# Optimization experiments

Hardware: AMD Instinct MI355X
Metric: run time of the kernel (lower is better)

Reference implementation:

```python
import jax, jax.numpy as jnp
import numpy as np

N_NODES = 100000
N_EDGES = 3200000
NEG_SLOPE = 0.2  # PyG GATConv default


def _gat_conv(x, src, dst, W, a_src, a_dst, b, num_nodes):
    # x: [N, Fin]; src/dst: [E'] (self-loops already appended)
    h = x @ W                                   # [N, Fout]
    alpha_src = h @ a_src                       # [N]
    alpha_dst = h @ a_dst                       # [N]
    e = jax.nn.leaky_relu(alpha_src[src] + alpha_dst[dst], NEG_SLOPE)  # [E']
    # segment softmax over incoming edges of each destination node
    e_max = jax.ops.segment_max(e, dst, num_segments=num_nodes)
    e_exp = jnp.exp(e - e_max[dst])
    denom = jax.ops.segment_sum(e_exp, dst, num_segments=num_nodes)
    alpha = e_exp / (denom[dst] + 1e-16)        # [E']
    out = jax.ops.segment_sum(h[src] * alpha[:, None], dst, num_segments=num_nodes)
    return out + b


def setup_inputs() -> dict:
    key = jax.random.key(0)
    ks = jax.random.split(key, 10)
    x = jax.random.normal(ks[0], (N_NODES, 1), jnp.float32)
    edge_index = jax.random.randint(ks[1], (2, N_EDGES), 0, N_NODES, dtype=jnp.int64)
    s1 = 1.0  # glorot-ish scales
    return {
        "x": x,
        "edge_index": edge_index,
        "W1": jax.random.normal(ks[2], (1, 20), jnp.float32) * s1,
        "a_src1": jax.random.normal(ks[3], (20,), jnp.float32) * 0.3,
        "a_dst1": jax.random.normal(ks[4], (20,), jnp.float32) * 0.3,
        "b1": jnp.zeros((20,), jnp.float32),
        "W2": jax.random.normal(ks[5], (20, 20), jnp.float32) * (1.0 / np.sqrt(20.0)),
        "a_src2": jax.random.normal(ks[6], (20,), jnp.float32) * 0.3,
        "a_dst2": jax.random.normal(ks[7], (20,), jnp.float32) * 0.3,
        "b2": jnp.zeros((20,), jnp.float32),
        "Wl": jax.random.normal(ks[8], (20, 1), jnp.float32) * (1.0 / np.sqrt(20.0)),
        "bl": jnp.zeros((1,), jnp.float32),
    }


def reference(x, edge_index, W1, a_src1, a_dst1, b1, W2, a_src2, a_dst2, b2, Wl, bl):
    n = x.shape[0]
    loop = jnp.arange(n, dtype=edge_index.dtype)
    src = jnp.concatenate([edge_index[0], loop])  # add_self_loops=True
    dst = jnp.concatenate([edge_index[1], loop])
    h = _gat_conv(x, src, dst, W1, a_src1, a_dst1, b1, n)
    h = jax.nn.relu(h)
    h = _gat_conv(h, src, dst, W2, a_src2, a_dst2, b2, n)
    h = jax.nn.relu(h)
    return h @ Wl + bl  # [N, 1]
```

## Files before the change

kernel.cpp:

```cpp
#include <hip/hip_runtime.h>
#include <hip/hip_fp16.h>

#define FDIM 20
#define NSLOPE 0.2f
#define BSHIFT 7
#define BSIZE 128
#define BCAP 4800
#define MAXBUCK 800
#define PGRID 512
#define HSTRIDE 24
#define ABLK 512
#define ITP 4
#define CHCAP 6272
#define OFFSTRIDE 132

__device__ __forceinline__ float lrelu(float v) { return v > 0.f ? v : NSLOPE * v; }

__global__ void __launch_bounds__(1024)
k_part(const int* __restrict__ ei, int E, int nbuck,
       const float* __restrict__ x, const float* __restrict__ W1,
       const float* __restrict__ a_src, const float* __restrict__ a_dst,
       float2* __restrict__ PX, float* __restrict__ AD,
       int* __restrict__ gcur, int* __restrict__ slab, int N)
{
    __shared__ int hist[MAXBUCK];
    __shared__ int lofs[MAXBUCK];
    __shared__ int gbase[MAXBUCK];
    __shared__ int sbuf[CHCAP];
    __shared__ unsigned short sbk[CHCAP];
    __shared__ int wsum[16];
    const int tid = threadIdx.x;

    {
        int g = blockIdx.x * 1024 + tid;
        if (g < N) {
            float cs = 0.f, cd = 0.f;
#pragma unroll
            for (int f = 0; f < FDIM; ++f) {
                float w = W1[f]; cs += w * a_src[f]; cd += w * a_dst[f];
            }
            float xv = x[g];
            PX[g] = make_float2(xv * cs, xv);
            AD[g] = xv * cd;
        }
    }

    const int chunk = (E + PGRID - 1) / PGRID;
    const int c0 = blockIdx.x * chunk;
    const int c1 = min(c0 + chunk, E);
    for (int t = tid; t < nbuck; t += 1024) hist[t] = 0;
    __syncthreads();

    int ent[2 * ITP], meta[2 * ITP];
#pragma unroll
    for (int it = 0; it < ITP; ++it) {
        int i = c0 + 2 * (tid + (it << 10));
        const int k0 = 2 * it, k1 = 2 * it + 1;
        meta[k0] = -1; meta[k1] = -1;
        if (i + 1 < c1) {
            int2 s2 = *(const int2*)(ei + i);
            int2 d2 = *(const int2*)(ei + E + i);
            int bA = d2.x >> BSHIFT, bB = d2.y >> BSHIFT;
            int lpA = atomicAdd(&hist[bA], 1);
            int lpB = atomicAdd(&hist[bB], 1);
            ent[k0]  = (s2.x << BSHIFT) | (d2.x & (BSIZE - 1));
            meta[k0] = (lpA << 10) | bA;
            ent[k1]  = (s2.y << BSHIFT) | (d2.y & (BSIZE - 1));
            meta[k1] = (lpB << 10) | bB;
        } else if (i < c1) {
            int s = ei[i], d = ei[E + i];
            int b = d >> BSHIFT;
            int lp = atomicAdd(&hist[b], 1);
            ent[k0]  = (s << BSHIFT) | (d & (BSIZE - 1));
            meta[k0] = (lp << 10) | b;
        }
    }
    __syncthreads();

    int myc = 0;
    if (tid < nbuck) {
        myc = hist[tid];
        gbase[tid] = myc ? atomicAdd(gcur + tid, myc) : 0;
    }
    int inc = myc;
#pragma unroll
    for (int o = 1; o < 64; o <<= 1) {
        int t = __shfl_up(inc, o);
        if ((tid & 63) >= o) inc += t;
    }
    if ((tid & 63) == 63) wsum[tid >> 6] = inc;
    __syncthreads();
    if (tid < 16) {
        int v = wsum[tid];
        int e = v;
#pragma unroll
        for (int o = 1; o < 16; o <<= 1) {
            int t = __shfl_up(e, o);
            if (tid >= o) e += t;
        }
        wsum[tid] = e - v;
    }
    __syncthreads();
    if (tid < nbuck) lofs[tid] = inc - myc + wsum[tid >> 6];
    __syncthreads();

#pragma unroll
    for (int k = 0; k < 2 * ITP; ++k) {
        int m = meta[k];
        if (m >= 0) {
            int b  = m & 1023;
            int lp = m >> 10;
            int pos = lofs[b] + lp;
            sbuf[pos] = ent[k];
            sbk[pos]  = (unsigned short)b;
        }
    }
    __syncthreads();

    const int cnt = c1 - c0;
    for (int i = tid; i < cnt; i += 1024) {
        int b  = sbk[i];
        int gp = gbase[b] + (i - lofs[b]);
        if (gp < BCAP) slab[(size_t)b * BCAP + gp] = sbuf[i];
    }
}

__device__ __forceinline__ void sort_bucket(const int* __restrict__ sp, int cnt,
                                            int* __restrict__ sedge,
                                            int* __restrict__ off,
                                            int* __restrict__ cur)
{
    const int tid = threadIdx.x;
    if (tid < BSIZE + 1) off[tid] = 0;
    __syncthreads();
    for (int i = tid; i < cnt; i += ABLK)
        atomicAdd(&off[(sp[i] & (BSIZE - 1)) + 1], 1);
    __syncthreads();
    if (tid < 64) {
        int a = off[2 * tid + 1];
        int c = off[2 * tid + 2];
        int s = a + c;
#pragma unroll
        for (int o = 1; o < 64; o <<= 1) {
            int t = __shfl_up(s, o);
            if (tid >= o) s += t;
        }
        int ex = s - a - c;
        off[2 * tid]     = ex;
        off[2 * tid + 1] = ex + a;
        cur[2 * tid]     = ex;
        cur[2 * tid + 1] = ex + a;
        if (tid == 63) off[BSIZE] = s;
    }
    __syncthreads();
    for (int i = tid; i < cnt; i += ABLK) {
        int e = sp[i];
        int pos = atomicAdd(&cur[e & (BSIZE - 1)], 1);
        sedge[pos] = e >> BSHIFT;
    }
    __syncthreads();
}

__global__ void __launch_bounds__(ABLK)
k_agg1(const int* __restrict__ gcur, const int* __restrict__ slab,
       const float2* __restrict__ PX, const float* __restrict__ AD,
       const float* __restrict__ W1, const float* __restrict__ b1,
       const float* __restrict__ W2,
       const float* __restrict__ as2w, const float* __restrict__ ad2w,
       __half* __restrict__ H, float* __restrict__ AD2,
       int* __restrict__ sedge_g, int* __restrict__ off_g, int N)
{
    __shared__ int sedge[BCAP];
    __shared__ int off[BSIZE + 1], cur[BSIZE];
    __shared__ float sAD[BSIZE];
    __shared__ float sW1[FDIM], sb1[FDIM], sW2[FDIM * FDIM], sas[FDIM], sad[FDIM];
    const int tid = threadIdx.x;
    const int b = blockIdx.x;
    const int dbase = b << BSHIFT;
    if (tid < BSIZE) { int d = dbase + tid; sAD[tid] = (d < N) ? AD[d] : 0.f; }
    for (int t = tid; t < FDIM * FDIM; t += ABLK) sW2[t] = W2[t];
    if (tid >= 480 && tid < 480 + FDIM) {
        int k = tid - 480;
        sW1[k] = W1[k]; sb1[k] = b1[k]; sas[k] = as2w[k]; sad[k] = ad2w[k];
    }
    const int cnt = min(gcur[b], BCAP);
    sort_bucket(slab + (size_t)b * BCAP, cnt, sedge, off, cur);

    for (int i = tid; i < cnt; i += ABLK) sedge_g[(size_t)b * BCAP + i] = sedge[i];
    if (tid <= BSIZE) off_g[b * OFFSTRIDE + tid] = off[tid];

    const int dl = tid >> 2, sub = tid & 3;
    const float adv = sAD[dl];
    float den = 0.f, sx = 0.f;
    const int e1 = off[dl + 1];
#pragma unroll 4
    for (int j = off[dl] + sub; j < e1; j += 4) {
        int s = sedge[j];
        float2 p = PX[s];
        float w = __expf(lrelu(p.x + adv));
        den += w; sx += w * p.y;
    }
    den += __shfl_xor(den, 1); den += __shfl_xor(den, 2);
    sx  += __shfl_xor(sx, 1);  sx  += __shfl_xor(sx, 2);
    const int d = dbase + dl;
    if (d < N) {
        float2 p = PX[d];
        float w = __expf(lrelu(p.x + adv));
        den += w; sx += w * p.y;
        float sv = sx / (den + 1e-16f);
        float tk[FDIM];
#pragma unroll
        for (int k = 0; k < FDIM; ++k) {
            float tv = sv * sW1[k] + sb1[k];
            tk[k] = tv > 0.f ? tv : 0.f;
        }
        const int fbase = sub << 3;
        const int nf = (sub < 2) ? 8 : (sub == 2 ? 4 : 0);
        float hv[8];
        float pas = 0.f, pad = 0.f;
#pragma unroll
        for (int t = 0; t < 8; ++t) {
            float hsum = 0.f;
            if (t < nf) {
#pragma unroll
                for (int k = 0; k < FDIM; ++k)
                    hsum += tk[k] * sW2[k * FDIM + fbase + t];
                pas += hsum * sas[fbase + t];
                pad += hsum * sad[fbase + t];
            }
            hv[t] = hsum;
        }
        pas += __shfl_xor(pas, 1); pas += __shfl_xor(pas, 2);
        pad += __shfl_xor(pad, 1); pad += __shfl_xor(pad, 2);
        __half2 p01 = __halves2half2(__float2half(hv[0]), __float2half(hv[1]));
        __half2 p23 = __halves2half2(__float2half(hv[2]), __float2half(hv[3]));
        __half2 p45 = __halves2half2(__float2half(hv[4]), __float2half(hv[5]));
        __half2 p67 = __halves2half2(__float2half(hv[6]), __float2half(hv[7]));
        uint4 q;
        q.x = *(unsigned*)&p01; q.y = *(unsigned*)&p23;
        q.z = *(unsigned*)&p45; q.w = *(unsigned*)&p67;
        if (sub == 2) { q.z = __float_as_uint(pas); q.w = 0u; }
        if (sub < 3) ((uint4*)(H + (size_t)d * HSTRIDE))[sub] = q;
        else AD2[d] = pad;
    }
}

__global__ void __launch_bounds__(ABLK)
k_agg2(const int* __restrict__ gcur, const int* __restrict__ sedge_g,
       const int* __restrict__ off_g,
       const __half* __restrict__ H, const float* __restrict__ AD2,
       const float* __restrict__ b2, const float* __restrict__ Wl,
       const float* __restrict__ bl,
       float* __restrict__ out, int N)
{
    __shared__ int sedge[BCAP];
    __shared__ int off[BSIZE + 1];
    __shared__ float sAD[BSIZE];
    __shared__ float sb2[FDIM], sWl[FDIM];
    const int tid = threadIdx.x;
    const int b = blockIdx.x;
    const int dbase = b << BSHIFT;
    if (tid < BSIZE) { int d = dbase + tid; sAD[tid] = (d < N) ? AD2[d] : 0.f; }
    if (tid >= 480 && tid < 480 + FDIM) {
        int k = tid - 480;
        sb2[k] = b2[k]; sWl[k] = Wl[k];
    }
    const int cnt = min(gcur[b], BCAP);
    for (int i = tid; i < cnt; i += ABLK) sedge[i] = sedge_g[(size_t)b * BCAP + i];
    if (tid <= BSIZE) off[tid] = off_g[b * OFFSTRIDE + tid];
    __syncthreads();

    const int dl = tid >> 2, sub = tid & 3;
    const float adv = sAD[dl];
    float den = 0.f;
    float acc[FDIM];
#pragma unroll
    for (int k = 0; k < FDIM; ++k) acc[k] = 0.f;
    const int e1 = off[dl + 1];
#pragma unroll 4
    for (int j = off[dl] + sub; j < e1; j += 4) {
        int s = sedge[j];
        const uint4* rp = (const uint4*)(H + (size_t)s * HSTRIDE);
        uint4 a = rp[0];
        uint4 bb = rp[1];
        uint4 c = rp[2];
        float w = __expf(lrelu(__uint_as_float(c.z) + adv));
        den += w;
        float2 f;
        f = __half22float2(*(__half2*)&a.x);  acc[0]  += w * f.x; acc[1]  += w * f.y;
        f = __half22float2(*(__half2*)&a.y);  acc[2]  += w * f.x; acc[3]  += w * f.y;
        f = __half22float2(*(__half2*)&a.z);  acc[4]  += w * f.x; acc[5]  += w * f.y;
        f = __half22float2(*(__half2*)&a.w);  acc[6]  += w * f.x; acc[7]  += w * f.y;
        f = __half22float2(*(__half2*)&bb.x); acc[8]  += w * f.x; acc[9]  += w * f.y;
        f = __half22float2(*(__half2*)&bb.y); acc[10] += w * f.x; acc[11] += w * f.y;
        f = __half22float2(*(__half2*)&bb.z); acc[12] += w * f.x; acc[13] += w * f.y;
        f = __half22float2(*(__half2*)&bb.w); acc[14] += w * f.x; acc[15] += w * f.y;
        f = __half22float2(*(__half2*)&c.x);  acc[16] += w * f.x; acc[17] += w * f.y;
        f = __half22float2(*(__half2*)&c.y);  acc[18] += w * f.x; acc[19] += w * f.y;
    }
    den += __shfl_xor(den, 1); den += __shfl_xor(den, 2);
#pragma unroll
    for (int k = 0; k < FDIM; ++k) {
        acc[k] += __shfl_xor(acc[k], 1);
        acc[k] += __shfl_xor(acc[k], 2);
    }
    const int d = dbase + dl;
    if (sub == 0 && d < N) {
        const uint4* rp = (const uint4*)(H + (size_t)d * HSTRIDE);
        uint4 a = rp[0], bb = rp[1], c = rp[2];
        float w = __expf(lrelu(__uint_as_float(c.z) + adv));
        den += w;
        float hv[FDIM];
        float2 f;
        f = __half22float2(*(__half2*)&a.x);  hv[0]  = f.x; hv[1]  = f.y;
        f = __half22float2(*(__half2*)&a.y);  hv[2]  = f.x; hv[3]  = f.y;
        f = __half22float2(*(__half2*)&a.z);  hv[4]  = f.x; hv[5]  = f.y;
        f = __half22float2(*(__half2*)&a.w);  hv[6]  = f.x; hv[7]  = f.y;
        f = __half22float2(*(__half2*)&bb.x); hv[8]  = f.x; hv[9]  = f.y;
        f = __half22float2(*(__half2*)&bb.y); hv[10] = f.x; hv[11] = f.y;
        f = __half22float2(*(__half2*)&bb.z); hv[12] = f.x; hv[13] = f.y;
        f = __half22float2(*(__half2*)&bb.w); hv[14] = f.x; hv[15] = f.y;
        f = __half22float2(*(__half2*)&c.x);  hv[16] = f.x; hv[17] = f.y;
        f = __half22float2(*(__half2*)&c.y);  hv[18] = f.x; hv[19] = f.y;
        float inv = 1.f / (den + 1e-16f);
        float r = 0.f;
#pragma unroll
        for (int k = 0; k < FDIM; ++k) {
            float v = (acc[k] + w * hv[k]) * inv + sb2[k];
            v = v > 0.f ? v : 0.f;
            r += v * sWl[k];
        }
        out[d] = r + bl[0];
    }
}

extern "C" void kernel_launch(void* const* d_in, const int* in_sizes, int n_in,
                              void* d_out, int out_size, void* d_ws, size_t ws_size,
                              hipStream_t stream)
{
    const float* x      = (const float*)d_in[0];
    const int*   ei     = (const int*)d_in[1];
    const float* W1     = (const float*)d_in[2];
    const float* a_src1 = (const float*)d_in[3];
    const float* a_dst1 = (const float*)d_in[4];
    const float* b1     = (const float*)d_in[5];
    const float* W2     = (const float*)d_in[6];
    const float* a_src2 = (const float*)d_in[7];
    const float* a_dst2 = (const float*)d_in[8];
    const float* b2     = (const float*)d_in[9];
    const float* Wl     = (const float*)d_in[10];
    const float* bl     = (const float*)d_in[11];
    float* out = (float*)d_out;

    const int N = in_sizes[0];
    const int E = in_sizes[1] / 2;
    const int NBUCK = (N + BSIZE - 1) >> BSHIFT;

    __half* H    = (__half*)d_ws;
    float2* PX   = (float2*)(H + (size_t)N * HSTRIDE);
    float*  AD   = (float*)(PX + N);
    float*  AD2  = AD + N;
    int*  gcur   = (int*)(AD2 + N);
    int*  slab   = gcur + MAXBUCK;
    int*  sedge_g = slab + (size_t)MAXBUCK * BCAP;
    int*  off_g   = sedge_g + (size_t)MAXBUCK * BCAP;

    hipMemsetAsync(gcur, 0, MAXBUCK * sizeof(int), stream);
    k_part<<<PGRID, 1024, 0, stream>>>(ei, E, NBUCK, x, W1, a_src1, a_dst1,
                                       PX, AD, gcur, slab, N);
    k_agg1<<<NBUCK, ABLK, 0, stream>>>(gcur, slab, PX, AD, W1, b1, W2,
                                       a_src2, a_dst2, H, AD2, sedge_g, off_g, N);
    k_agg2<<<NBUCK, ABLK, 0, stream>>>(gcur, sedge_g, off_g, H, AD2, b2, Wl, bl,
                                       out, N);
}
```

Before: 173.9 us.

## Halve destination bucket size and use eight lanes per destination node

Shrinks destination buckets from 128 to 64 nodes, which doubles the bucket count (so the partition kernel now handles two buckets per thread and widens its meta encoding) and makes each aggregation block serve 64 nodes. Each destination now gets 8 lanes instead of 4 to walk its incoming edges, with an extra shuffle reduction step. The aim is more blocks and more lanes per node, giving more memory-level parallelism in the gather loops. In exchange there are twice as many blocks with their own setup and sort cost, more global bucket atomics, and half the lanes in the layer-2 feature stage now do redundant work.

```diff
diff --git a/kernel.cpp b/kernel.cpp
--- a/kernel.cpp
+++ b/kernel.cpp
@@ -3,16 +3,16 @@
 
 #define FDIM 20
 #define NSLOPE 0.2f
-#define BSHIFT 7
-#define BSIZE 128
-#define BCAP 4800
-#define MAXBUCK 800
+#define BSHIFT 6
+#define BSIZE 64
+#define BCAP 2560
+#define MAXBUCK 1600
 #define PGRID 512
 #define HSTRIDE 24
 #define ABLK 512
 #define ITP 4
 #define CHCAP 6272
-#define OFFSTRIDE 132
+#define OFFSTRIDE 68
 
 __device__ __forceinline__ float lrelu(float v) { return v > 0.f ? v : NSLOPE * v; }
 
@@ -64,25 +64,33 @@
             int lpA = atomicAdd(&hist[bA], 1);
             int lpB = atomicAdd(&hist[bB], 1);
             ent[k0]  = (s2.x << BSHIFT) | (d2.x & (BSIZE - 1));
-            meta[k0] = (lpA << 10) | bA;
+            meta[k0] = (lpA << 11) | bA;
             ent[k1]  = (s2.y << BSHIFT) | (d2.y & (BSIZE - 1));
-            meta[k1] = (lpB << 10) | bB;
+            meta[k1] = (lpB << 11) | bB;
         } else if (i < c1) {
             int s = ei[i], d = ei[E + i];
             int b = d >> BSHIFT;
             int lp = atomicAdd(&hist[b], 1);
             ent[k0]  = (s << BSHIFT) | (d & (BSIZE - 1));
-            meta[k0] = (lp << 10) | b;
-        }
-    }
-    __syncthreads();
-
-    int myc = 0;
-    if (tid < nbuck) {
-        myc = hist[tid];
-        gbase[tid] = myc ? atomicAdd(gcur + tid, myc) : 0;
-    }
-    int inc = myc;
+            meta[k0] = (lp << 11) | b;
+        }
+    }
+    __syncthreads();
+
+    int a = 0, c = 0;
+    {
+        int b0 = 2 * tid, b1 = 2 * tid + 1;
+        if (b0 < nbuck) {
+            a = hist[b0];
+            gbase[b0] = a ? atomicAdd(gcur + b0, a) : 0;
+        }
+        if (b1 < nbuck) {
+            c = hist[b1];
+            gbase[b1] = c ? atomicAdd(gcur + b1, c) : 0;
+        }
+    }
+    int s = a + c;
+    int inc = s;
 #pragma unroll
     for (int o = 1; o < 64; o <<= 1) {
         int t = __shfl_up(inc, o);
@@ -101,15 +109,20 @@
         wsum[tid] = e - v;
     }
     __syncthreads();
-    if (tid < nbuck) lofs[tid] = inc - myc + wsum[tid >> 6];
+    {
+        int ex = inc - s + wsum[tid >> 6];
+        int b0 = 2 * tid, b1 = 2 * tid + 1;
+        if (b0 < nbuck) lofs[b0] = ex;
+        if (b1 < nbuck) lofs[b1] = ex + a;
+    }
     __syncthreads();
 
 #pragma unroll
     for (int k = 0; k < 2 * ITP; ++k) {
         int m = meta[k];
         if (m >= 0) {
-            int b  = m & 1023;
-            int lp = m >> 10;
+            int b  = m & 2047;
+            int lp = m >> 11;
             int pos = lofs[b] + lp;
             sbuf[pos] = ent[k];
             sbk[pos]  = (unsigned short)b;
@@ -137,20 +150,15 @@
         atomicAdd(&off[(sp[i] & (BSIZE - 1)) + 1], 1);
     __syncthreads();
     if (tid < 64) {
-        int a = off[2 * tid + 1];
-        int c = off[2 * tid + 2];
-        int s = a + c;
+        int v = off[tid + 1];
+        int s = v;
 #pragma unroll
         for (int o = 1; o < 64; o <<= 1) {
             int t = __shfl_up(s, o);
             if (tid >= o) s += t;
         }
-        int ex = s - a - c;
-        off[2 * tid]     = ex;
-        off[2 * tid + 1] = ex + a;
-        cur[2 * tid]     = ex;
-        cur[2 * tid + 1] = ex + a;
-        if (tid == 63) off[BSIZE] = s;
+        off[tid + 1] = s;
+        cur[tid] = s - v;
     }
     __syncthreads();
     for (int i = tid; i < cnt; i += ABLK) {
@@ -189,19 +197,19 @@
     for (int i = tid; i < cnt; i += ABLK) sedge_g[(size_t)b * BCAP + i] = sedge[i];
     if (tid <= BSIZE) off_g[b * OFFSTRIDE + tid] = off[tid];
 
-    const int dl = tid >> 2, sub = tid & 3;
+    const int dl = tid >> 3, sub = tid & 7;
     const float adv = sAD[dl];
     float den = 0.f, sx = 0.f;
     const int e1 = off[dl + 1];
 #pragma unroll 4
-    for (int j = off[dl] + sub; j < e1; j += 4) {
+    for (int j = off[dl] + sub; j < e1; j += 8) {
         int s = sedge[j];
         float2 p = PX[s];
         float w = __expf(lrelu(p.x + adv));
         den += w; sx += w * p.y;
     }
-    den += __shfl_xor(den, 1); den += __shfl_xor(den, 2);
-    sx  += __shfl_xor(sx, 1);  sx  += __shfl_xor(sx, 2);
+    den += __shfl_xor(den, 1); den += __shfl_xor(den, 2); den += __shfl_xor(den, 4);
+    sx  += __shfl_xor(sx, 1);  sx  += __shfl_xor(sx, 2);  sx  += __shfl_xor(sx, 4);
     const int d = dbase + dl;
     if (d < N) {
         float2 p = PX[d];
@@ -214,7 +222,7 @@
             float tv = sv * sW1[k] + sb1[k];
             tk[k] = tv > 0.f ? tv : 0.f;
         }
-        const int fbase = sub << 3;
+        const int fbase = (sub & 3) << 3;
         const int nf = (sub < 2) ? 8 : (sub == 2 ? 4 : 0);
         float hv[8];
         float pas = 0.f, pad = 0.f;
@@ -230,8 +238,8 @@
             }
             hv[t] = hsum;
         }
-        pas += __shfl_xor(pas, 1); pas += __shfl_xor(pas, 2);
-        pad += __shfl_xor(pad, 1); pad += __shfl_xor(pad, 2);
+        pas += __shfl_xor(pas, 1); pas += __shfl_xor(pas, 2); pas += __shfl_xor(pas, 4);
+        pad += __shfl_xor(pad, 1); pad += __shfl_xor(pad, 2); pad += __shfl_xor(pad, 4);
         __half2 p01 = __halves2half2(__float2half(hv[0]), __float2half(hv[1]));
         __half2 p23 = __halves2half2(__float2half(hv[2]), __float2half(hv[3]));
         __half2 p45 = __halves2half2(__float2half(hv[4]), __float2half(hv[5]));
@@ -241,7 +249,7 @@
         q.z = *(unsigned*)&p45; q.w = *(unsigned*)&p67;
         if (sub == 2) { q.z = __float_as_uint(pas); q.w = 0u; }
         if (sub < 3) ((uint4*)(H + (size_t)d * HSTRIDE))[sub] = q;
-        else AD2[d] = pad;
+        else if (sub == 3) AD2[d] = pad;
     }
 }
 
@@ -270,7 +278,7 @@
     if (tid <= BSIZE) off[tid] = off_g[b * OFFSTRIDE + tid];
     __syncthreads();
 
-    const int dl = tid >> 2, sub = tid & 3;
+    const int dl = tid >> 3, sub = tid & 7;
     const float adv = sAD[dl];
     float den = 0.f;
     float acc[FDIM];
@@ -278,7 +286,7 @@
     for (int k = 0; k < FDIM; ++k) acc[k] = 0.f;
     const int e1 = off[dl + 1];
 #pragma unroll 4
-    for (int j = off[dl] + sub; j < e1; j += 4) {
+    for (int j = off[dl] + sub; j < e1; j += 8) {
         int s = sedge[j];
         const uint4* rp = (const uint4*)(H + (size_t)s * HSTRIDE);
         uint4 a = rp[0];
@@ -298,11 +306,12 @@
         f = __half22float2(*(__half2*)&c.x);  acc[16] += w * f.x; acc[17] += w * f.y;
         f = __half22float2(*(__half2*)&c.y);  acc[18] += w * f.x; acc[19] += w * f.y;
     }
-    den += __shfl_xor(den, 1); den += __shfl_xor(den, 2);
+    den += __shfl_xor(den, 1); den += __shfl_xor(den, 2); den += __shfl_xor(den, 4);
 #pragma unroll
     for (int k = 0; k < FDIM; ++k) {
         acc[k] += __shfl_xor(acc[k], 1);
         acc[k] += __shfl_xor(acc[k], 2);
+        acc[k] += __shfl_xor(acc[k], 4);
     }
     const int d = dbase + dl;
     if (sub == 0 && d < N) {
```

Measured after the change: 185.5 us. +6.7%, slower.
